# Kernel optimization log

Measured on AMD Instinct MI355X. Metric: run time of the kernel, lower is better.

Reference implementation:

```python
import jax, jax.numpy as jnp
import numpy as np

B, C, H, W = 8, 384, 32, 32
NUM_HEADS = 8
HEAD_DIM = C // NUM_HEADS
HIDDEN = max(32, C // 2)


def setup_inputs() -> dict:
    key = jax.random.key(0)
    ks = jax.random.split(key, 6)
    s = lambda fan_in: 1.0 / np.sqrt(fan_in)
    return {
        "x": jax.random.normal(ks[0], (B, C, H, W), dtype=jnp.float32),
        "qkv_w": jax.random.normal(ks[1], (C, 3 * C), dtype=jnp.float32) * s(C),
        "qkv_b": jnp.zeros((3 * C,), dtype=jnp.float32),
        "proj_w": jax.random.normal(ks[2], (C, C), dtype=jnp.float32) * s(C),
        "proj_b": jnp.zeros((C,), dtype=jnp.float32),
        "mlp_w1": jax.random.normal(ks[3], (2, HIDDEN), dtype=jnp.float32) * s(2),
        "mlp_b1": jnp.zeros((HIDDEN,), dtype=jnp.float32),
        "mlp_w2": jax.random.normal(ks[4], (HIDDEN, NUM_HEADS), dtype=jnp.float32) * s(HIDDEN),
        "mlp_b2": jnp.zeros((NUM_HEADS,), dtype=jnp.float32),
    }


def _relative_bias(h, w, mlp_w1, mlp_b1, mlp_w2, mlp_b2):
    ch = jnp.arange(h, dtype=jnp.float32)
    cw = jnp.arange(w, dtype=jnp.float32)
    coords = jnp.stack(jnp.meshgrid(ch, cw, indexing="ij"), axis=-1).reshape(-1, 2)  # [N,2]
    rel = coords[:, None, :] - coords[None, :, :]  # [N,N,2]
    denom = jnp.array([max(h - 1, 1), max(w - 1, 1)], dtype=jnp.float32)
    rel = rel / denom
    hidden = jax.nn.gelu(rel @ mlp_w1 + mlp_b1, approximate=False)
    bias = hidden @ mlp_w2 + mlp_b2  # [N,N,heads]
    return jnp.transpose(bias, (2, 0, 1))  # [heads,N,N]


def reference(x, qkv_w, qkv_b, proj_w, proj_b, mlp_w1, mlp_b1, mlp_w2, mlp_b2):
    b, c, h, w = x.shape
    n = h * w
    tokens = x.reshape(b, c, n).transpose(0, 2, 1)  # [B,N,C]
    qkv = (tokens @ qkv_w + qkv_b).reshape(b, n, 3, NUM_HEADS, HEAD_DIM)
    qkv = jnp.transpose(qkv, (2, 0, 3, 1, 4))  # [3,B,h,N,d]
    q, k, v = qkv[0], qkv[1], qkv[2]
    scale = HEAD_DIM ** -0.5
    attn = jnp.einsum("bhnd,bhmd->bhnm", q * scale, k)
    attn = attn + _relative_bias(h, w, mlp_w1, mlp_b1, mlp_w2, mlp_b2)[None]
    attn = jax.nn.softmax(attn, axis=-1)
    out = jnp.einsum("bhnm,bhmd->bhnd", attn, v)
    out = out.transpose(0, 2, 1, 3).reshape(b, n, c)
    out = out @ proj_w + proj_b
    return out.transpose(0, 2, 1).reshape(b, c, h, w)
```

## Files before the change

### kernel.cpp

```cpp
#include <hip/hip_runtime.h>
#include <hip/hip_bf16.h>
#include <math.h>

#define BB 8
#define CC 384
#define NT 1024
#define NHEAD 8
#define HD 48
#define HIDDEN 192
#define THREEC 1152

typedef short short8 __attribute__((ext_vector_type(8)));
typedef short short4v __attribute__((ext_vector_type(4)));
typedef float f32x4 __attribute__((ext_vector_type(4)));
typedef unsigned int uint2v __attribute__((ext_vector_type(2)));
typedef unsigned int uint4v __attribute__((ext_vector_type(4)));

static __device__ __forceinline__ short bf16bits(float v) {
  __hip_bfloat16 h = __float2bfloat16(v);
  return *(short*)&h;
}
static __device__ __forceinline__ unsigned pk2(float a, float b) {
  return __builtin_amdgcn_perm(__float_as_uint(b) + 0x8000u,
                               __float_as_uint(a) + 0x8000u, 0x07060302u);
}
static __device__ __forceinline__ void lds_dma16(const void* g, void* l) {
  __builtin_amdgcn_global_load_lds((const __attribute__((address_space(1))) unsigned*)g,
                                   (__attribute__((address_space(3))) unsigned*)l, 16, 0, 0);
}
static __device__ __forceinline__ void pl16swap(unsigned& a, unsigned& b) {
  asm("v_permlane16_swap_b32 %0, %1" : "+v"(a), "+v"(b));
}

__global__ __launch_bounds__(256) void k_prep(
    const float* __restrict__ x, const float* __restrict__ qkv_w,
    const float* __restrict__ proj_w,
    const float* __restrict__ w1, const float* __restrict__ b1,
    const float* __restrict__ w2, const float* __restrict__ b2,
    __hip_bfloat16* __restrict__ xt, __hip_bfloat16* __restrict__ wtq,
    __hip_bfloat16* __restrict__ wtp, float* __restrict__ tab) {
  const int bid = blockIdx.x;
  const int tid = threadIdx.x;
  if (bid >= 3648) {
    int g = (bid - 3648) * 256 + tid;
    int p = g >> 3, jc = g & 7;
    if (p >= 63 * 63) return;
    float rh = (float)(p / 63 - 31) * (1.0f / 31.0f);
    float rw = (float)(p % 63 - 31) * (1.0f / 31.0f);
    float acc[8] = {0.f, 0.f, 0.f, 0.f, 0.f, 0.f, 0.f, 0.f};
    const int j0 = jc * 24;
#pragma unroll 4
    for (int j = j0; j < j0 + 24; j++) {
      float pre = fmaf(rh, w1[j], fmaf(rw, w1[HIDDEN + j], b1[j]));
      float gl = 0.5f * pre * (1.0f + erff(pre * 0.70710678118654752f));
#pragma unroll
      for (int h = 0; h < 8; h++) acc[h] = fmaf(gl, w2[j * 8 + h], acc[h]);
    }
#pragma unroll
    for (int msk = 1; msk <= 4; msk <<= 1)
#pragma unroll
      for (int h = 0; h < 8; h++) acc[h] += __shfl_xor(acc[h], msk);
    if (jc == 0) {
#pragma unroll
      for (int h = 0; h < 8; h++)
        tab[h * 3969 + p] = (acc[h] + b2[h]) * 1.4426950408889634f;
    }
    return;
  }
  const float* src;
  __hip_bfloat16* dst;
  int R, C, r0, c0;
  if (bid < 3072) {
    int zi = bid / 384, rem = bid % 384;
    R = 384; C = 1024;
    r0 = (rem / 32) * 32; c0 = (rem % 32) * 32;
    src = x + (size_t)zi * R * C;
    dst = xt + (size_t)zi * R * C;
  } else if (bid < 3504) {
    int i = bid - 3072;
    R = 384; C = 1152;
    r0 = (i / 36) * 32; c0 = (i % 36) * 32;
    src = qkv_w; dst = wtq;
  } else {
    int i = bid - 3504;
    R = 384; C = 384;
    r0 = (i / 12) * 32; c0 = (i % 12) * 32;
    src = proj_w; dst = wtp;
  }
  __shared__ float t[32][33];
#pragma unroll
  for (int e = 0; e < 4; e++) {
    int i = tid + e * 256;
    int r = i >> 5, c = i & 31;
    t[r][c] = src[(size_t)(r0 + r) * C + c0 + c];
  }
  __syncthreads();
#pragma unroll
  for (int e = 0; e < 4; e++) {
    int i = tid + e * 256;
    int c = i >> 5, r = i & 31;
    dst[(size_t)(c0 + c) * R + r0 + r] = __float2bfloat16(t[r][c]);
  }
}

__global__ __launch_bounds__(512) void k_qkv_mfma(
    const __hip_bfloat16* __restrict__ xt,
    const __hip_bfloat16* __restrict__ wtq,
    const float* __restrict__ qkv_b,
    __hip_bfloat16* __restrict__ Qb,
    __hip_bfloat16* __restrict__ Kb,
    __hip_bfloat16* __restrict__ Vt)
{
  __shared__ __align__(16) char smem[34816];
  short* As = (short*)smem;
  short* Bs = (short*)(smem + 8192);
  float* Vf = (float*)smem;
  const int n0 = blockIdx.x * 128;
  const int m0 = blockIdx.y * 64;
  const int tid = threadIdx.x;
  const int wv = tid >> 6, lane = tid & 63, quad = lane >> 4, lq = lane & 15;
  const int wc = wv >> 2, wm = wv & 3;
  const int lrow = lane >> 3;
  const int gsw = ((lane & 7) ^ lrow) * 8;
  const int sw0 = (quad ^ (lq & 7)) * 8;
  const int sw1 = sw0 ^ 32;
  f32x4 acc[4];
#pragma unroll
  for (int nt = 0; nt < 4; nt++) acc[nt] = (f32x4){0.f, 0.f, 0.f, 0.f};
  for (int kk = 0; kk < CC; kk += 64) {
    __syncthreads();
    for (int c = wv; c < 24; c += 8) {
      if (c < 8)
        lds_dma16((const short*)xt + (size_t)(m0 + c * 8 + lrow) * 384 + kk + gsw,
                  smem + c * 1024);
      else
        lds_dma16((const short*)wtq + (size_t)(n0 + (c - 8) * 8 + lrow) * 384 + kk + gsw,
                  smem + 8192 + (c - 8) * 1024);
    }
    __syncthreads();
    short8 a0 = *(const short8*)(As + (wm * 16 + lq) * 64 + sw0);
    short8 a1 = *(const short8*)(As + (wm * 16 + lq) * 64 + sw1);
    __builtin_amdgcn_s_setprio(1);
#pragma unroll
    for (int nt = 0; nt < 4; nt++) {
      acc[nt] = __builtin_amdgcn_mfma_f32_16x16x32_bf16(
          a0, *(const short8*)(Bs + (wc * 64 + nt * 16 + lq) * 64 + sw0), acc[nt], 0, 0, 0);
      acc[nt] = __builtin_amdgcn_mfma_f32_16x16x32_bf16(
          a1, *(const short8*)(Bs + (wc * 64 + nt * 16 + lq) * 64 + sw1), acc[nt], 0, 0, 0);
    }
    __builtin_amdgcn_s_setprio(0);
  }
  __syncthreads();
  const float qscale = 0.14433756729740643f * 1.4426950408889634f;
  const float sc = (n0 < 384) ? qscale : 1.0f;
#pragma unroll
  for (int nt = 0; nt < 4; nt++) {
    float bias = qkv_b[n0 + wc * 64 + nt * 16 + lq];
#pragma unroll
    for (int r = 0; r < 4; r++)
      Vf[(wc * 64 + nt * 16 + lq) * 68 + wm * 16 + quad * 4 + r] = (acc[nt][r] + bias) * sc;
  }
  __syncthreads();
  if (n0 >= 768) {
    int ch = tid & 127, grp = tid >> 7;
    int cg = n0 - 768 + ch;
    int head = cg / 48, d = cg - head * 48;
    int b = m0 >> 10;
    int n = (m0 & 1023) + grp * 16;
    const float* src = Vf + ch * 68 + grp * 16;
    short o16[16];
#pragma unroll
    for (int k = 0; k < 16; k++) o16[k] = bf16bits(src[k]);
    short* dst = (short*)Vt + ((size_t)(b * 8 + head) * 48 + d) * 1024 + n;
    *(short8*)dst = *(short8*)o16;
    *(short8*)(dst + 8) = *(short8*)(o16 + 8);
  } else {
    const int which = n0 >= 384;
    short* Out = which ? (short*)Kb : (short*)Qb;
    int n_l = tid & 63, seg = tid >> 6;
    int rr0 = (n0 - which * 384) + seg * 16;
    int head = rr0 / 48, d0 = rr0 - head * 48;
    int b = m0 >> 10;
    int n_g = (m0 & 1023) + n_l;
    const float* src = Vf + (seg * 16) * 68 + n_l;
    short o16[16];
#pragma unroll
    for (int k = 0; k < 16; k++) o16[k] = bf16bits(src[k * 68]);
    short* dst = Out + (((size_t)(b * 8 + head) << 10) + n_g) * 64 + d0;
    *(short8*)dst = *(short8*)o16;
    *(short8*)(dst + 8) = *(short8*)(o16 + 8);
    if (d0 == 0) {
      short8 z = (short8){0, 0, 0, 0, 0, 0, 0, 0};
      *(short8*)(dst + 48) = z;
      *(short8*)(dst + 56) = z;
    }
  }
}

#define K0_OFF 0
#define V0_OFF 16384
#define TR_OFF 28672
#define SMEM_SZ 32768
__global__ __launch_bounds__(512, 4) void k_flash(
    const __hip_bfloat16* __restrict__ Qb, const __hip_bfloat16* __restrict__ Kb,
    const __hip_bfloat16* __restrict__ Vt, const float* __restrict__ tab,
    __hip_bfloat16* __restrict__ ATb)
{
  __shared__ __align__(16) char smem[SMEM_SZ];
  float* Os = (float*)smem;

  const int tid = threadIdx.x;
  const int wv = tid >> 6, lane = tid & 63, quad = lane >> 4, lq = lane & 15;
  const int bh = blockIdx.x;
  const int q0 = blockIdx.y * 128;
  const int b = bh >> 3, h = bh & 7;
  const int inr0 = q0 >> 5;

  const int nrow = q0 + wv * 16 + lq;
  const int jnr = nrow & 31;
  const int rloc = (nrow >> 5) - inr0 + 1;
  const int tbase = rloc * 63 + jnr + 31 - 4 * quad;

  short8 qf0, qf1;
  {
    const short* qp = (const short*)Qb + ((size_t)(bh << 10) + nrow) * 64;
    qf0 = *(const short8*)(qp + quad * 8);
    qf1 = *(const short8*)(qp + 32 + quad * 8);
  }
  short8 onesv;
#pragma unroll
  for (int j = 0; j < 8; j++) onesv[j] = (short)0x3F80;

  f32x4 O[4];
#pragma unroll
  for (int dt = 0; dt < 4; dt++) O[dt] = (f32x4){0.f, 0.f, 0.f, 0.f};

  const short* kgp = (const short*)Kb + ((size_t)(bh << 10)) * 64;
  const short* vgp = (const short*)Vt + (size_t)bh * 48 * 1024;
  const float* tabg = tab + h * 3969;
  const int lrow = lane >> 3;
  const int gsw = ((lane & 7) ^ lrow) * 8;
  const int sw0 = (quad ^ (lq & 7)) * 8;
  const int sw1 = sw0 ^ 32;
  const int vq = ((quad & 1) << 1) | (quad >> 1);
  const int swv0 = (vq ^ (lq & 7)) * 8;
  const int swv1 = swv0 ^ 32;

  for (int c = wv; c < 16; c += 8) {
    if (c < 8)
      lds_dma16(kgp + (size_t)(c * 8 + lrow) * 64 + gsw, smem + K0_OFF + c * 1024);
    else if (c < 14)
      lds_dma16(vgp + (size_t)((c - 8) * 8 + lrow) * 1024 + gsw,
                smem + V0_OFF + (c - 8) * 1024);
    else if (c == 14)
      lds_dma16(tabg + (inr0 + 30) * 63 + lane * 4, smem + TR_OFF);
    else
      lds_dma16(tabg + (inr0 + 30) * 63 + 256 + lane * 4, smem + TR_OFF + 1024);
  }

  for (int it = 0; it < 16; it++) {
    const int m0 = it * 64;
    const int buf = it & 1;
    __syncthreads();
    if (it < 15) {
      const int nbuf = buf ^ 1;
      const int mn = m0 + 64;
      for (int c = wv; c < 16; c += 8) {
        if (c < 8)
          lds_dma16(kgp + (size_t)(mn + c * 8 + lrow) * 64 + gsw,
                    smem + K0_OFF + nbuf * 8192 + c * 1024);
        else if (c < 14)
          lds_dma16(vgp + (size_t)((c - 8) * 8 + lrow) * 1024 + mn + gsw,
                    smem + V0_OFF + nbuf * 6144 + (c - 8) * 1024);
        else if (c == 14)
          lds_dma16(tabg + (inr0 + 28 - 2 * it) * 63 + lane * 4,
                    smem + TR_OFF + nbuf * 2048);
        else
          lds_dma16(tabg + (inr0 + 28 - 2 * it) * 63 + 256 + lane * 4,
                    smem + TR_OFF + nbuf * 2048 + 1024);
      }
    }
    const short* Kl = (const short*)(smem + K0_OFF + buf * 8192);
    const short* Vl = (const short*)(smem + V0_OFF + buf * 6144);
    const float* Tl = (const float*)(smem + TR_OFF + buf * 2048);

    float s[4][4];
    __builtin_amdgcn_s_setprio(1);
#pragma unroll
    for (int nt = 0; nt < 4; nt++) {
      const float* tn = Tl + tbase - (nt >= 2 ? 63 : 0) - (nt & 1) * 16;
      f32x4 c;
      c[0] = tn[0]; c[1] = tn[-1]; c[2] = tn[-2]; c[3] = tn[-3];
      c = __builtin_amdgcn_mfma_f32_16x16x32_bf16(
          *(const short8*)(Kl + (nt * 16 + lq) * 64 + sw0), qf0, c, 0, 0, 0);
      c = __builtin_amdgcn_mfma_f32_16x16x32_bf16(
          *(const short8*)(Kl + (nt * 16 + lq) * 64 + sw1), qf1, c, 0, 0, 0);
#pragma unroll
      for (int r = 0; r < 4; r++) s[nt][r] = c[r];
    }
    __builtin_amdgcn_s_setprio(0);
#pragma unroll
    for (int nt = 0; nt < 4; nt++)
#pragma unroll
      for (int r = 0; r < 4; r++) s[nt][r] = exp2f(s[nt][r]);
    uint4v p0, p1;
    {
      unsigned a, bb_;
      a = pk2(s[0][0], s[0][1]); bb_ = pk2(s[1][0], s[1][1]);
      pl16swap(a, bb_); p0[0] = a; p0[2] = bb_;
      a = pk2(s[0][2], s[0][3]); bb_ = pk2(s[1][2], s[1][3]);
      pl16swap(a, bb_); p0[1] = a; p0[3] = bb_;
      a = pk2(s[2][0], s[2][1]); bb_ = pk2(s[3][0], s[3][1]);
      pl16swap(a, bb_); p1[0] = a; p1[2] = bb_;
      a = pk2(s[2][2], s[2][3]); bb_ = pk2(s[3][2], s[3][3]);
      pl16swap(a, bb_); p1[1] = a; p1[3] = bb_;
    }
    short8 pf0 = *(short8*)&p0;
    short8 pf1 = *(short8*)&p1;
    __builtin_amdgcn_s_setprio(1);
#pragma unroll
    for (int dt = 0; dt < 3; dt++)
      O[dt] = __builtin_amdgcn_mfma_f32_16x16x32_bf16(
          *(const short8*)(Vl + (dt * 16 + lq) * 64 + swv0), pf0, O[dt], 0, 0, 0);
    O[3] = __builtin_amdgcn_mfma_f32_16x16x32_bf16(onesv, pf0, O[3], 0, 0, 0);
#pragma unroll
    for (int dt = 0; dt < 3; dt++)
      O[dt] = __builtin_amdgcn_mfma_f32_16x16x32_bf16(
          *(const short8*)(Vl + (dt * 16 + lq) * 64 + swv1), pf1, O[dt], 0, 0, 0);
    O[3] = __builtin_amdgcn_mfma_f32_16x16x32_bf16(onesv, pf1, O[3], 0, 0, 0);
    __builtin_amdgcn_s_setprio(0);
  }
  float inv = 1.0f / O[3][0];
  __syncthreads();
#pragma unroll
  for (int dt = 0; dt < 3; dt++)
#pragma unroll
    for (int r = 0; r < 4; r++)
      Os[(wv * 16 + lq) * 52 + dt * 16 + quad * 4 + r] = O[dt][r] * inv;
  __syncthreads();
  {
    int row = tid >> 2, cg = (tid & 3) * 12;
    const float* src = Os + row * 52 + cg;
    short outp[12];
#pragma unroll
    for (int k = 0; k < 12; k++) outp[k] = bf16bits(src[k]);
    short* dst = (short*)ATb + ((size_t)(b << 10) + q0 + row) * 384 + h * 48 + cg;
    *(short4v*)dst = *(short4v*)outp;
    *(short4v*)(dst + 4) = *(short4v*)(outp + 4);
    *(short4v*)(dst + 8) = *(short4v*)(outp + 8);
  }
}

__global__ __launch_bounds__(256) void k_proj_mfma(
    const __hip_bfloat16* __restrict__ ATb,
    const __hip_bfloat16* __restrict__ wtp,
    const float* __restrict__ pb, float* __restrict__ out) {
  __shared__ __align__(16) char smem[16384];
  short* As = (short*)smem;
  short* Bs = (short*)(smem + 8192);
  const int c0 = blockIdx.x * 64;
  const int n0 = blockIdx.y * 64;
  const int b = blockIdx.z;
  const int tid = threadIdx.x;
  const int wv = tid >> 6, lane = tid & 63, quad = lane >> 4, lq = lane & 15;
  const int lrow = lane >> 3;
  const int gsw = ((lane & 7) ^ lrow) * 8;
  const int sw0 = (quad ^ (lq & 7)) * 8;
  const int sw1 = sw0 ^ 32;
  f32x4 acc[4];
#pragma unroll
  for (int nt = 0; nt < 4; nt++) acc[nt] = (f32x4){0.f, 0.f, 0.f, 0.f};
  for (int kk = 0; kk < CC; kk += 64) {
    __syncthreads();
    for (int c = wv; c < 16; c += 4) {
      if (c < 8)
        lds_dma16((const short*)wtp + (size_t)(c0 + c * 8 + lrow) * 384 + kk + gsw,
                  smem + c * 1024);
      else
        lds_dma16((const short*)ATb + ((size_t)(b << 10) + n0 + (c - 8) * 8 + lrow) * 384 + kk + gsw,
                  smem + 8192 + (c - 8) * 1024);
    }
    __syncthreads();
    short8 a0 = *(const short8*)(As + (wv * 16 + lq) * 64 + sw0);
    short8 a1 = *(const short8*)(As + (wv * 16 + lq) * 64 + sw1);
#pragma unroll
    for (int nt = 0; nt < 4; nt++) {
      acc[nt] = __builtin_amdgcn_mfma_f32_16x16x32_bf16(
          a0, *(const short8*)(Bs + (nt * 16 + lq) * 64 + sw0), acc[nt], 0, 0, 0);
      acc[nt] = __builtin_amdgcn_mfma_f32_16x16x32_bf16(
          a1, *(const short8*)(Bs + (nt * 16 + lq) * 64 + sw1), acc[nt], 0, 0, 0);
    }
  }
#pragma unroll
  for (int nt = 0; nt < 4; nt++) {
    int n = n0 + nt * 16 + lq;
#pragma unroll
    for (int r = 0; r < 4; r++) {
      int c = c0 + wv * 16 + quad * 4 + r;
      out[((size_t)b * 384 + c) * 1024 + n] = acc[nt][r] + pb[c];
    }
  }
}

extern "C" void kernel_launch(void* const* d_in, const int* in_sizes, int n_in,
                              void* d_out, int out_size, void* d_ws, size_t ws_size,
                              hipStream_t stream) {
  const float* x = (const float*)d_in[0];
  const float* qkv_w = (const float*)d_in[1];
  const float* qkv_b = (const float*)d_in[2];
  const float* proj_w = (const float*)d_in[3];
  const float* proj_b = (const float*)d_in[4];
  const float* w1 = (const float*)d_in[5];
  const float* b1 = (const float*)d_in[6];
  const float* w2 = (const float*)d_in[7];
  const float* b2 = (const float*)d_in[8];
  float* out = (float*)d_out;

  char* w = (char*)d_ws;
  __hip_bfloat16* xt = (__hip_bfloat16*)w;   w += (size_t)8192 * 384 * 2;
  __hip_bfloat16* wtq = (__hip_bfloat16*)w;  w += (size_t)1152 * 384 * 2;
  __hip_bfloat16* wtp = (__hip_bfloat16*)w;  w += (size_t)384 * 384 * 2;
  __hip_bfloat16* Qb = (__hip_bfloat16*)w;   w += (size_t)64 * 1024 * 64 * 2;
  __hip_bfloat16* Kb = (__hip_bfloat16*)w;   w += (size_t)64 * 1024 * 64 * 2;
  __hip_bfloat16* Vt = (__hip_bfloat16*)w;   w += (size_t)64 * 48 * 1024 * 2;
  __hip_bfloat16* ATb = (__hip_bfloat16*)w;  w += (size_t)8192 * 384 * 2;
  float* tab = (float*)w;                    w += (size_t)8 * 3969 * 4 + 1024;

  k_prep<<<dim3(3773), dim3(256), 0, stream>>>(x, qkv_w, proj_w, w1, b1, w2, b2,
                                               xt, wtq, wtp, tab);
  k_qkv_mfma<<<dim3(9, 128), dim3(512), 0, stream>>>(xt, wtq, qkv_b, Qb, Kb, Vt);
  k_flash<<<dim3(64, 8), dim3(512), 0, stream>>>(Qb, Kb, Vt, tab, ATb);
  k_proj_mfma<<<dim3(6, 16, 8), dim3(256), 0, stream>>>(ATb, wtp, proj_b, out);
}
```

Measured before the change: 166.1 us.

## Split flash attention over two key halves and combine partials in separate kernel

The attention kernel now splits the key dimension into two halves via a third grid dimension. Each half writes unnormalized fp32 partial outputs and row sums, and a new combine kernel adds them, normalizes, and writes bf16. This doubles the block count to improve CU occupancy and latency hiding. In exchange it adds a kernel launch and substantial fp32 intermediate memory traffic.

```diff
diff --git a/kernel.cpp b/kernel.cpp
--- a/kernel.cpp
+++ b/kernel.cpp
@@ -204,16 +204,18 @@
 __global__ __launch_bounds__(512, 4) void k_flash(
     const __hip_bfloat16* __restrict__ Qb, const __hip_bfloat16* __restrict__ Kb,
     const __hip_bfloat16* __restrict__ Vt, const float* __restrict__ tab,
-    __hip_bfloat16* __restrict__ ATb)
+    float* __restrict__ Opart,
+    float* __restrict__ Lpart)
 {
   __shared__ __align__(16) char smem[SMEM_SZ];
-  float* Os = (float*)smem;
 
   const int tid = threadIdx.x;
   const int wv = tid >> 6, lane = tid & 63, quad = lane >> 4, lq = lane & 15;
   const int bh = blockIdx.x;
   const int q0 = blockIdx.y * 128;
-  const int b = bh >> 3, h = bh & 7;
+  const int z = blockIdx.z;
+  const int kt0 = z * 8;
+  const int h = bh & 7;
   const int inr0 = q0 >> 5;
 
   const int nrow = q0 + wv * 16 + lq;
@@ -248,21 +250,23 @@
 
   for (int c = wv; c < 16; c += 8) {
     if (c < 8)
-      lds_dma16(kgp + (size_t)(c * 8 + lrow) * 64 + gsw, smem + K0_OFF + c * 1024);
+      lds_dma16(kgp + (size_t)(kt0 * 64 + c * 8 + lrow) * 64 + gsw,
+                smem + K0_OFF + c * 1024);
     else if (c < 14)
-      lds_dma16(vgp + (size_t)((c - 8) * 8 + lrow) * 1024 + gsw,
+      lds_dma16(vgp + (size_t)((c - 8) * 8 + lrow) * 1024 + kt0 * 64 + gsw,
                 smem + V0_OFF + (c - 8) * 1024);
     else if (c == 14)
-      lds_dma16(tabg + (inr0 + 30) * 63 + lane * 4, smem + TR_OFF);
+      lds_dma16(tabg + (inr0 + 30 - 2 * kt0) * 63 + lane * 4, smem + TR_OFF);
     else
-      lds_dma16(tabg + (inr0 + 30) * 63 + 256 + lane * 4, smem + TR_OFF + 1024);
-  }
-
-  for (int it = 0; it < 16; it++) {
-    const int m0 = it * 64;
+      lds_dma16(tabg + (inr0 + 30 - 2 * kt0) * 63 + 256 + lane * 4, smem + TR_OFF + 1024);
+  }
+
+  for (int it = 0; it < 8; it++) {
+    const int kt = kt0 + it;
+    const int m0 = kt * 64;
     const int buf = it & 1;
     __syncthreads();
-    if (it < 15) {
+    if (it < 7) {
       const int nbuf = buf ^ 1;
       const int mn = m0 + 64;
       for (int c = wv; c < 16; c += 8) {
@@ -273,10 +277,10 @@
           lds_dma16(vgp + (size_t)((c - 8) * 8 + lrow) * 1024 + mn + gsw,
                     smem + V0_OFF + nbuf * 6144 + (c - 8) * 1024);
         else if (c == 14)
-          lds_dma16(tabg + (inr0 + 28 - 2 * it) * 63 + lane * 4,
+          lds_dma16(tabg + (inr0 + 28 - 2 * kt) * 63 + lane * 4,
                     smem + TR_OFF + nbuf * 2048);
         else
-          lds_dma16(tabg + (inr0 + 28 - 2 * it) * 63 + 256 + lane * 4,
+          lds_dma16(tabg + (inr0 + 28 - 2 * kt) * 63 + 256 + lane * 4,
                     smem + TR_OFF + nbuf * 2048 + 1024);
       }
     }
@@ -330,25 +334,37 @@
     O[3] = __builtin_amdgcn_mfma_f32_16x16x32_bf16(onesv, pf1, O[3], 0, 0, 0);
     __builtin_amdgcn_s_setprio(0);
   }
-  float inv = 1.0f / O[3][0];
-  __syncthreads();
-#pragma unroll
-  for (int dt = 0; dt < 3; dt++)
-#pragma unroll
-    for (int r = 0; r < 4; r++)
-      Os[(wv * 16 + lq) * 52 + dt * 16 + quad * 4 + r] = O[dt][r] * inv;
-  __syncthreads();
   {
-    int row = tid >> 2, cg = (tid & 3) * 12;
-    const float* src = Os + row * 52 + cg;
-    short outp[12];
-#pragma unroll
-    for (int k = 0; k < 12; k++) outp[k] = bf16bits(src[k]);
-    short* dst = (short*)ATb + ((size_t)(b << 10) + q0 + row) * 384 + h * 48 + cg;
-    *(short4v*)dst = *(short4v*)outp;
-    *(short4v*)(dst + 4) = *(short4v*)(outp + 4);
-    *(short4v*)(dst + 8) = *(short4v*)(outp + 8);
-  }
+    const int q = q0 + wv * 16 + lq;
+    float* op = Opart + (((size_t)(z * 64 + bh) << 10) + q) * 48 + quad * 4;
+#pragma unroll
+    for (int dt = 0; dt < 3; dt++) *(f32x4*)(op + dt * 16) = O[dt];
+    if (quad == 0) Lpart[((size_t)(z * 64 + bh) << 10) + q] = O[3][0];
+  }
+}
+
+__global__ __launch_bounds__(256) void k_comb(
+    const float* __restrict__ Opart, const float* __restrict__ Lpart,
+    __hip_bfloat16* __restrict__ ATb) {
+  const int bh = blockIdx.x, b = bh >> 3, h = bh & 7;
+  const int q = blockIdx.y * 64 + (threadIdx.x >> 2);
+  const int cg = (threadIdx.x & 3) * 12;
+  const size_t r0 = (((size_t)bh << 10) + q) * 48 + cg;
+  const size_t r1 = (((size_t)(64 + bh) << 10) + q) * 48 + cg;
+  const float inv = 1.0f / (Lpart[((size_t)bh << 10) + q] +
+                            Lpart[(size_t)65536 + ((size_t)bh << 10) + q]);
+  short outp[12];
+#pragma unroll
+  for (int g = 0; g < 3; g++) {
+    f32x4 a = *(const f32x4*)(Opart + r0 + g * 4);
+    f32x4 c = *(const f32x4*)(Opart + r1 + g * 4);
+#pragma unroll
+    for (int r = 0; r < 4; r++) outp[g * 4 + r] = bf16bits((a[r] + c[r]) * inv);
+  }
+  short* dst = (short*)ATb + (((size_t)b << 10) + q) * 384 + h * 48 + cg;
+  *(short4v*)dst = *(short4v*)outp;
+  *(short4v*)(dst + 4) = *(short4v*)(outp + 4);
+  *(short4v*)(dst + 8) = *(short4v*)(outp + 8);
 }
 
 __global__ __launch_bounds__(256) void k_proj_mfma(
@@ -425,10 +441,13 @@
   __hip_bfloat16* Vt = (__hip_bfloat16*)w;   w += (size_t)64 * 48 * 1024 * 2;
   __hip_bfloat16* ATb = (__hip_bfloat16*)w;  w += (size_t)8192 * 384 * 2;
   float* tab = (float*)w;                    w += (size_t)8 * 3969 * 4 + 1024;
+  float* Opart = (float*)w;                  w += (size_t)2 * 64 * 1024 * 48 * 4;
+  float* Lpart = (float*)w;                  w += (size_t)2 * 64 * 1024 * 4;
 
   k_prep<<<dim3(3773), dim3(256), 0, stream>>>(x, qkv_w, proj_w, w1, b1, w2, b2,
                                                xt, wtq, wtp, tab);
   k_qkv_mfma<<<dim3(9, 128), dim3(512), 0, stream>>>(xt, wtq, qkv_b, Qb, Kb, Vt);
-  k_flash<<<dim3(64, 8), dim3(512), 0, stream>>>(Qb, Kb, Vt, tab, ATb);
+  k_flash<<<dim3(64, 8, 2), dim3(512), 0, stream>>>(Qb, Kb, Vt, tab, Opart, Lpart);
+  k_comb<<<dim3(64, 16), dim3(256), 0, stream>>>(Opart, Lpart, ATb);
   k_proj_mfma<<<dim3(6, 16, 8), dim3(256), 0, stream>>>(ATb, wtp, proj_b, out);
 }
```

New measurement: 174.6 us. +5.1%, slower.
